# Kernel tuning notes

Measured on AMD Instinct MI355X. Metric: run time of the kernel, lower is better.

The kernel has to match this reference:

```python
import jax, jax.numpy as jnp
import numpy as np

N_NODES = 100000
N_EDGES = 1600000
IN_F = 32
D = 128
OUT = 16


def setup_inputs() -> dict:
    key = jax.random.key(0)
    ks = jax.random.split(key, 12)
    inp = {
        "x": jax.random.normal(ks[0], (N_NODES, IN_F), dtype=jnp.float32),
        "edge_index": jax.random.randint(ks[1], (2, N_EDGES), 0, N_NODES, dtype=jnp.int64),
        # node embedder (Linear IN_F -> D)
        "W_emb": jax.random.normal(ks[2], (IN_F, D), dtype=jnp.float32) / np.sqrt(IN_F),
        "b_emb": jnp.zeros((D,), dtype=jnp.float32),
        # conv1: relation weight, root weight, bias
        "W1_rel": jax.random.normal(ks[3], (D, D), dtype=jnp.float32) / np.sqrt(D),
        "W1_root": jax.random.normal(ks[4], (D, D), dtype=jnp.float32) / np.sqrt(D),
        "b1": jnp.zeros((D,), dtype=jnp.float32),
        # conv2
        "W2_rel": jax.random.normal(ks[5], (D, D), dtype=jnp.float32) / np.sqrt(D),
        "W2_root": jax.random.normal(ks[6], (D, D), dtype=jnp.float32) / np.sqrt(D),
        "b2": jnp.zeros((D,), dtype=jnp.float32),
        # final layer D -> OUT
        "W_out": jax.random.normal(ks[7], (D, OUT), dtype=jnp.float32) / np.sqrt(D),
        "b_out": jnp.zeros((OUT,), dtype=jnp.float32),
    }
    return inp


def _rgcn_mean(h, src, dst, W_rel, W_root, b):
    # FastRGCNConv with num_relations=1, aggr='mean':
    # out_i = mean_{j -> i}(h_j @ W_rel) + h_i @ W_root + b
    msg = h[src] @ W_rel  # [E, D] gather + per-edge transform
    agg = jax.ops.segment_sum(msg, dst, num_segments=N_NODES)
    cnt = jax.ops.segment_sum(jnp.ones((dst.shape[0],), dtype=h.dtype), dst,
                              num_segments=N_NODES)
    agg = agg / jnp.maximum(cnt, 1.0)[:, None]  # scatter-mean; isolated nodes -> 0
    return agg + h @ W_root + b


def reference(x, edge_index, W_emb, b_emb, W1_rel, W1_root, b1,
              W2_rel, W2_root, b2, W_out, b_out):
    src, dst = edge_index[0], edge_index[1]
    h = x @ W_emb + b_emb                                   # node embed
    h = jax.nn.relu(_rgcn_mean(h, src, dst, W1_rel, W1_root, b1))
    h = jax.nn.relu(_rgcn_mean(h, src, dst, W2_rel, W2_root, b2))
    return h @ W_out + b_out                                # [N_NODES, OUT]
```

## Files before the change

kernel.cpp:

```cpp
#include <hip/hip_runtime.h>
#include <hip/hip_bf16.h>

#define N_NODES 100000
#define N_EDGES 1600000
#define IN_F    32
#define D       128
#define OUT_F   16
#define NB      ((N_NODES + 255) / 256)
#define NSLICE  8
#define SLICE_NODES (N_NODES / NSLICE)
#define FILL_CHUNKS 512

typedef __attribute__((ext_vector_type(8))) short  bf16x8;
typedef __attribute__((ext_vector_type(4))) float  f32x4;

__device__ __forceinline__ unsigned short f2bf(float x) {
    unsigned u = __float_as_uint(x);
    unsigned r = (u + 0x7FFFu + ((u >> 16) & 1u)) >> 16;
    return (unsigned short)r;
}
__device__ __forceinline__ float bf2f(unsigned short h) {
    return __uint_as_float(((unsigned)h) << 16);
}

__global__ __launch_bounds__(256) void k_embed(const float* __restrict__ x,
                                               const float* __restrict__ W,
                                               const float* __restrict__ b,
                                               unsigned short* __restrict__ h_hi,
                                               unsigned short* __restrict__ h_lo) {
    __shared__ float xs[16][IN_F];
    const int base = blockIdx.x * 16;

    if (threadIdx.x < 128) {
        int r = threadIdx.x >> 3, c4 = (threadIdx.x & 7) << 2;
        *reinterpret_cast<float4*>(&xs[r][c4]) =
            *reinterpret_cast<const float4*>(x + (long)(base + r) * IN_F + c4);
    }
    __syncthreads();

    const int nl   = threadIdx.x >> 4;
    const int col0 = (threadIdx.x & 15) << 3;

    float acc[8];
    {
        float4 b0 = *reinterpret_cast<const float4*>(b + col0);
        float4 b1 = *reinterpret_cast<const float4*>(b + col0 + 4);
        acc[0] = b0.x; acc[1] = b0.y; acc[2] = b0.z; acc[3] = b0.w;
        acc[4] = b1.x; acc[5] = b1.y; acc[6] = b1.z; acc[7] = b1.w;
    }
#pragma unroll
    for (int k = 0; k < IN_F; ++k) {
        const float xv = xs[nl][k];
        float4 w0 = *reinterpret_cast<const float4*>(W + k * D + col0);
        float4 w1 = *reinterpret_cast<const float4*>(W + k * D + col0 + 4);
        acc[0] += xv * w0.x; acc[1] += xv * w0.y; acc[2] += xv * w0.z; acc[3] += xv * w0.w;
        acc[4] += xv * w1.x; acc[5] += xv * w1.y; acc[6] += xv * w1.z; acc[7] += xv * w1.w;
    }

    unsigned short hh[8], ll[8];
#pragma unroll
    for (int j = 0; j < 8; ++j) {
        unsigned short h = f2bf(acc[j]);
        hh[j] = h;
        ll[j] = f2bf(acc[j] - bf2f(h));
    }
    long off = (long)(base + nl) * D + col0;
    *reinterpret_cast<bf16x8*>(h_hi + off) = *reinterpret_cast<bf16x8*>(hh);
    *reinterpret_cast<bf16x8*>(h_lo + off) = *reinterpret_cast<bf16x8*>(ll);
}

__global__ __launch_bounds__(256) void k_count(const int* __restrict__ dst,
                                               int* __restrict__ cnt) {
    const int slice = blockIdx.x & (NSLICE - 1);
    const int chunk = blockIdx.x >> 3;
    const int lo = slice * SLICE_NODES;
    const int hi = lo + SLICE_NODES;
    for (int e = chunk * 256 + threadIdx.x; e < N_EDGES; e += FILL_CHUNKS * 256) {
        int d = dst[e];
        if (d >= lo && d < hi) atomicAdd(&cnt[d], 1);
    }
}

__global__ __launch_bounds__(256) void k_scan1(const int* __restrict__ cnt,
                                               int* __restrict__ part,
                                               int* __restrict__ blockSums) {
    __shared__ int s[256];
    int i = blockIdx.x * 256 + threadIdx.x;
    int v = (i < N_NODES) ? cnt[i] : 0;
    s[threadIdx.x] = v;
    __syncthreads();
    for (int off = 1; off < 256; off <<= 1) {
        int x = (threadIdx.x >= off) ? s[threadIdx.x - off] : 0;
        __syncthreads();
        s[threadIdx.x] += x;
        __syncthreads();
    }
    if (i < N_NODES) part[i] = s[threadIdx.x] - v;
    if (threadIdx.x == 255) blockSums[blockIdx.x] = s[255];
}

__global__ __launch_bounds__(512) void k_scan2(int* __restrict__ blockSums) {
    __shared__ int s[512];
    int t = threadIdx.x;
    int v = (t < NB) ? blockSums[t] : 0;
    s[t] = v;
    __syncthreads();
    for (int off = 1; off < 512; off <<= 1) {
        int x = (t >= off) ? s[t - off] : 0;
        __syncthreads();
        s[t] += x;
        __syncthreads();
    }
    if (t < NB) blockSums[t] = s[t] - v;
}

__global__ __launch_bounds__(256) void k_scan3(int* __restrict__ offsets,
                                               const int* __restrict__ blockSums,
                                               int* __restrict__ cursor) {
    int i = blockIdx.x * 256 + threadIdx.x;
    if (i < N_NODES) {
        int o = offsets[i] + blockSums[blockIdx.x];
        offsets[i] = o;
        cursor[i]  = o;
    }
}

__global__ __launch_bounds__(256) void k_fill(const int* __restrict__ src,
                                              const int* __restrict__ dst,
                                              int* __restrict__ cursor,
                                              int* __restrict__ csr) {
    const int slice = blockIdx.x & (NSLICE - 1);
    const int chunk = blockIdx.x >> 3;
    const int lo = slice * SLICE_NODES;
    const int hi = lo + SLICE_NODES;
    for (int e = chunk * 256 + threadIdx.x; e < N_EDGES; e += FILL_CHUNKS * 256) {
        int d = dst[e];
        if (d >= lo && d < hi) {
            int p = atomicAdd(&cursor[d], 1);
            csr[p] = src[e];
        }
    }
}

__global__ __launch_bounds__(256) void k_wprep(const float* __restrict__ W1r,
                                               const float* __restrict__ W1o,
                                               const float* __restrict__ W2r,
                                               const float* __restrict__ W2o,
                                               unsigned short* __restrict__ wp) {
    int c = blockIdx.x * 256 + threadIdx.x;
    int layer = c >> 12;
    int ko = (c >> 7) & 31;
    int n = c & 127;
    const float* Wrel  = layer ? W2r : W1r;
    const float* Wroot = layer ? W2o : W1o;

    unsigned short hi[8], lo[8];
#pragma unroll
    for (int j = 0; j < 8; ++j) {
        int k = ko * 8 + j;
        float w = (k < D) ? Wrel[k * D + n] : Wroot[(k - D) * D + n];
        unsigned short h = f2bf(w);
        hi[j] = h;
        lo[j] = f2bf(w - bf2f(h));
    }
    unsigned short* base = wp + layer * 65536 + ((ko * 128 + n) << 3);
    *reinterpret_cast<bf16x8*>(base)         = *reinterpret_cast<bf16x8*>(hi);
    *reinterpret_cast<bf16x8*>(base + 32768) = *reinterpret_cast<bf16x8*>(lo);
}

template <bool LAST>
__global__ __launch_bounds__(512) void k_fused(const unsigned short* __restrict__ hin_hi,
                                               const unsigned short* __restrict__ hin_lo,
                                               const int* __restrict__ csr,
                                               const int* __restrict__ offsets,
                                               const int* __restrict__ cnt,
                                               const unsigned short* __restrict__ Wh,
                                               const unsigned short* __restrict__ Wl,
                                               const float* __restrict__ b,
                                               unsigned short* __restrict__ ho_hi,
                                               unsigned short* __restrict__ ho_lo,
                                               const float* __restrict__ Wout,
                                               const float* __restrict__ bout,
                                               float* __restrict__ outp) {
    __shared__ unsigned short Ahi[32 * 32 * 8];
    __shared__ unsigned short Alo[32 * 32 * 8];
    const int base = blockIdx.x * 32;
    const int tid  = threadIdx.x;

    {
        const int ko  = tid & 15;
        const int q8  = ko << 3;
        const int row = tid >> 4;
        const int node = base + row;
        const int beg = offsets[node];
        const int deg = cnt[node];
        const int end = beg + deg;

        float a0[8], a1[8];
#pragma unroll
        for (int j = 0; j < 8; ++j) { a0[j] = 0.f; a1[j] = 0.f; }

        int i = beg;
        for (; i + 3 < end; i += 4) {
            int s0 = csr[i], s1 = csr[i + 1], s2 = csr[i + 2], s3 = csr[i + 3];
            bf16x8 v0 = *reinterpret_cast<const bf16x8*>(hin_hi + (long)s0 * D + q8);
            bf16x8 v1 = *reinterpret_cast<const bf16x8*>(hin_hi + (long)s1 * D + q8);
            bf16x8 v2 = *reinterpret_cast<const bf16x8*>(hin_hi + (long)s2 * D + q8);
            bf16x8 v3 = *reinterpret_cast<const bf16x8*>(hin_hi + (long)s3 * D + q8);
#pragma unroll
            for (int j = 0; j < 8; ++j) {
                a0[j] += bf2f((unsigned short)v0[j]) + bf2f((unsigned short)v1[j]);
                a1[j] += bf2f((unsigned short)v2[j]) + bf2f((unsigned short)v3[j]);
            }
        }
        for (; i < end; ++i) {
            int s0 = csr[i];
            bf16x8 v0 = *reinterpret_cast<const bf16x8*>(hin_hi + (long)s0 * D + q8);
#pragma unroll
            for (int j = 0; j < 8; ++j) a0[j] += bf2f((unsigned short)v0[j]);
        }

        const float sc = 1.f / fmaxf((float)deg, 1.f);
        unsigned short hh[8], ll[8];
#pragma unroll
        for (int j = 0; j < 8; ++j) {
            float v = (a0[j] + a1[j]) * sc;
            unsigned short h = f2bf(v);
            hh[j] = h;
            ll[j] = f2bf(v - bf2f(h));
        }
        const int byteoff = ((ko * 32 + row) * 16) ^ ((ko & 7) << 4);
        *reinterpret_cast<bf16x8*>(reinterpret_cast<char*>(Ahi) + byteoff) =
            *reinterpret_cast<bf16x8*>(hh);
        *reinterpret_cast<bf16x8*>(reinterpret_cast<char*>(Alo) + byteoff) =
            *reinterpret_cast<bf16x8*>(ll);
    }

    {
        int ko16 = tid & 15;
        int row  = tid >> 4;
        long off = (long)(base + row) * D + ko16 * 8;
        bf16x8 vh = *reinterpret_cast<const bf16x8*>(hin_hi + off);
        bf16x8 vl = *reinterpret_cast<const bf16x8*>(hin_lo + off);
        int ko = 16 + ko16;
        int byteoff = ((ko * 32 + row) * 16) ^ ((ko & 7) << 4);
        *reinterpret_cast<bf16x8*>(reinterpret_cast<char*>(Ahi) + byteoff) = vh;
        *reinterpret_cast<bf16x8*>(reinterpret_cast<char*>(Alo) + byteoff) = vl;
    }
    __syncthreads();

    const int lane = tid & 63;
    const int wid  = tid >> 6;
    const int mw  = wid & 1;
    const int nwq = wid >> 1;
    const int l15 = lane & 15;
    const int l4  = lane >> 4;

    f32x4 acc[2];
#pragma unroll
    for (int ct = 0; ct < 2; ++ct) acc[ct] = (f32x4){0.f, 0.f, 0.f, 0.f};

    const int arow = mw * 16 + l15;

#pragma unroll
    for (int s = 0; s < 8; ++s) {
        const int ks = s * 4 + l4;
        const int abyte = ((ks * 32 + arow) * 16) ^ ((ks & 7) << 4);
        bf16x8 ah = *reinterpret_cast<const bf16x8*>(
                        reinterpret_cast<const char*>(Ahi) + abyte);
        bf16x8 al = *reinterpret_cast<const bf16x8*>(
                        reinterpret_cast<const char*>(Alo) + abyte);
#pragma unroll
        for (int ct = 0; ct < 2; ++ct) {
            const int colb = nwq * 32 + ct * 16 + l15;
            const long bidx = ((long)(ks * 128 + colb)) << 3;
            bf16x8 bh = *reinterpret_cast<const bf16x8*>(Wh + bidx);
            bf16x8 bl = *reinterpret_cast<const bf16x8*>(Wl + bidx);
            acc[ct] = __builtin_amdgcn_mfma_f32_16x16x32_bf16(ah, bh, acc[ct], 0, 0, 0);
            acc[ct] = __builtin_amdgcn_mfma_f32_16x16x32_bf16(al, bh, acc[ct], 0, 0, 0);
            acc[ct] = __builtin_amdgcn_mfma_f32_16x16x32_bf16(ah, bl, acc[ct], 0, 0, 0);
        }
    }

    if (!LAST) {
#pragma unroll
        for (int ct = 0; ct < 2; ++ct) {
            const int col = nwq * 32 + ct * 16 + l15;
            const float bv = b[col];
#pragma unroll
            for (int r = 0; r < 4; ++r) {
                long node = base + mw * 16 + l4 * 4 + r;
                float v = fmaxf(acc[ct][r] + bv, 0.f);
                unsigned short h = f2bf(v);
                ho_hi[node * D + col] = h;
                ho_lo[node * D + col] = f2bf(v - bf2f(h));
            }
        }
    } else {
        __syncthreads();
        float* hsm = reinterpret_cast<float*>(Ahi);
#pragma unroll
        for (int ct = 0; ct < 2; ++ct) {
            const int col = nwq * 32 + ct * 16 + l15;
            const float bv = b[col];
#pragma unroll
            for (int r = 0; r < 4; ++r) {
                int nl = mw * 16 + l4 * 4 + r;
                hsm[nl * D + ((col + 4 * nl) & 127)] = fmaxf(acc[ct][r] + bv, 0.f);
            }
        }
        __syncthreads();

        const int nl = tid >> 4;
        const int oo = tid & 15;
        float acc0 = bout[oo];
#pragma unroll 8
        for (int k = 0; k < D; ++k) {
            float hv = hsm[nl * D + ((k + 4 * nl) & 127)];
            acc0 += hv * Wout[k * OUT_F + oo];
        }
        outp[(long)(base + nl) * OUT_F + oo] = acc0;
    }
}

extern "C" void kernel_launch(void* const* d_in, const int* in_sizes, int n_in,
                              void* d_out, int out_size, void* d_ws, size_t ws_size,
                              hipStream_t stream) {
    const float* x      = (const float*)d_in[0];
    const int*   edge   = (const int*)d_in[1];
    const float* W_emb  = (const float*)d_in[2];
    const float* b_emb  = (const float*)d_in[3];
    const float* W1_rel = (const float*)d_in[4];
    const float* W1_root= (const float*)d_in[5];
    const float* b1     = (const float*)d_in[6];
    const float* W2_rel = (const float*)d_in[7];
    const float* W2_root= (const float*)d_in[8];
    const float* b2     = (const float*)d_in[9];
    const float* W_out  = (const float*)d_in[10];
    const float* b_out  = (const float*)d_in[11];
    float* out = (float*)d_out;

    const int* src = edge;
    const int* dst = edge + N_EDGES;

    const size_t ND = (size_t)N_NODES * D;

    unsigned short* hA_hi = (unsigned short*)d_ws;
    unsigned short* hA_lo = hA_hi + ND;
    unsigned short* hB_hi = hA_lo + ND;
    unsigned short* hB_lo = hB_hi + ND;
    int*   cnt     = (int*)(hB_lo + ND);
    int*   offsets = cnt + N_NODES;
    int*   cursor  = offsets + N_NODES;
    int*   bsums   = cursor + N_NODES;
    unsigned short* wpack = (unsigned short*)(bsums + 400);
    int*   csr     = (int*)(wpack + 4 * 32768);

    hipMemsetAsync(cnt, 0, N_NODES * sizeof(int), stream);
    k_count<<<NSLICE * FILL_CHUNKS, 256, 0, stream>>>(dst, cnt);
    k_scan1<<<NB, 256, 0, stream>>>(cnt, offsets, bsums);
    k_scan2<<<1, 512, 0, stream>>>(bsums);
    k_scan3<<<NB, 256, 0, stream>>>(offsets, bsums, cursor);
    k_fill<<<NSLICE * FILL_CHUNKS, 256, 0, stream>>>(src, dst, cursor, csr);
    k_wprep<<<32, 256, 0, stream>>>(W1_rel, W1_root, W2_rel, W2_root, wpack);

    k_embed<<<N_NODES / 16, 256, 0, stream>>>(x, W_emb, b_emb, hA_hi, hA_lo);

    k_fused<false><<<N_NODES / 32, 512, 0, stream>>>(
        hA_hi, hA_lo, csr, offsets, cnt,
        wpack, wpack + 32768, b1, hB_hi, hB_lo, nullptr, nullptr, nullptr);

    k_fused<true><<<N_NODES / 32, 512, 0, stream>>>(
        hB_hi, hB_lo, csr, offsets, cnt,
        wpack + 65536, wpack + 98304, b2, nullptr, nullptr, W_out, b_out, out);
}
```

Measured before the change: 460.9 us.

## Merge embed, count and weight-prep kernels; vectorize edge loads; software-pipeline gather

```diff
diff --git a/kernel.cpp b/kernel.cpp
--- a/kernel.cpp
+++ b/kernel.cpp
@@ -9,7 +9,12 @@
 #define NB      ((N_NODES + 255) / 256)
 #define NSLICE  8
 #define SLICE_NODES (N_NODES / NSLICE)
-#define FILL_CHUNKS 512
+
+#define NI4     (N_EDGES / 4)
+#define EBLK    ((NI4 + 1023) / 1024)
+#define NEMB    (N_NODES / 16)
+#define NCNT    (NSLICE * EBLK)
+#define NWP     32
 
 typedef __attribute__((ext_vector_type(8))) short  bf16x8;
 typedef __attribute__((ext_vector_type(4))) float  f32x4;
@@ -23,61 +28,107 @@
     return __uint_as_float(((unsigned)h) << 16);
 }
 
-__global__ __launch_bounds__(256) void k_embed(const float* __restrict__ x,
-                                               const float* __restrict__ W,
-                                               const float* __restrict__ b,
-                                               unsigned short* __restrict__ h_hi,
-                                               unsigned short* __restrict__ h_lo) {
-    __shared__ float xs[16][IN_F];
-    const int base = blockIdx.x * 16;
-
-    if (threadIdx.x < 128) {
-        int r = threadIdx.x >> 3, c4 = (threadIdx.x & 7) << 2;
-        *reinterpret_cast<float4*>(&xs[r][c4]) =
-            *reinterpret_cast<const float4*>(x + (long)(base + r) * IN_F + c4);
-    }
-    __syncthreads();
-
-    const int nl   = threadIdx.x >> 4;
-    const int col0 = (threadIdx.x & 15) << 3;
-
-    float acc[8];
-    {
-        float4 b0 = *reinterpret_cast<const float4*>(b + col0);
-        float4 b1 = *reinterpret_cast<const float4*>(b + col0 + 4);
-        acc[0] = b0.x; acc[1] = b0.y; acc[2] = b0.z; acc[3] = b0.w;
-        acc[4] = b1.x; acc[5] = b1.y; acc[6] = b1.z; acc[7] = b1.w;
-    }
-#pragma unroll
-    for (int k = 0; k < IN_F; ++k) {
-        const float xv = xs[nl][k];
-        float4 w0 = *reinterpret_cast<const float4*>(W + k * D + col0);
-        float4 w1 = *reinterpret_cast<const float4*>(W + k * D + col0 + 4);
-        acc[0] += xv * w0.x; acc[1] += xv * w0.y; acc[2] += xv * w0.z; acc[3] += xv * w0.w;
-        acc[4] += xv * w1.x; acc[5] += xv * w1.y; acc[6] += xv * w1.z; acc[7] += xv * w1.w;
-    }
-
-    unsigned short hh[8], ll[8];
-#pragma unroll
-    for (int j = 0; j < 8; ++j) {
-        unsigned short h = f2bf(acc[j]);
-        hh[j] = h;
-        ll[j] = f2bf(acc[j] - bf2f(h));
-    }
-    long off = (long)(base + nl) * D + col0;
-    *reinterpret_cast<bf16x8*>(h_hi + off) = *reinterpret_cast<bf16x8*>(hh);
-    *reinterpret_cast<bf16x8*>(h_lo + off) = *reinterpret_cast<bf16x8*>(ll);
-}
-
-__global__ __launch_bounds__(256) void k_count(const int* __restrict__ dst,
-                                               int* __restrict__ cnt) {
-    const int slice = blockIdx.x & (NSLICE - 1);
-    const int chunk = blockIdx.x >> 3;
-    const int lo = slice * SLICE_NODES;
-    const int hi = lo + SLICE_NODES;
-    for (int e = chunk * 256 + threadIdx.x; e < N_EDGES; e += FILL_CHUNKS * 256) {
-        int d = dst[e];
-        if (d >= lo && d < hi) atomicAdd(&cnt[d], 1);
+__global__ __launch_bounds__(256) void k_prep(const float* __restrict__ x,
+                                              const float* __restrict__ Wemb,
+                                              const float* __restrict__ bemb,
+                                              unsigned short* __restrict__ h_hi,
+                                              unsigned short* __restrict__ h_lo,
+                                              const int* __restrict__ dst,
+                                              int* __restrict__ cnt,
+                                              const float* __restrict__ W1r,
+                                              const float* __restrict__ W1o,
+                                              const float* __restrict__ W2r,
+                                              const float* __restrict__ W2o,
+                                              unsigned short* __restrict__ wp) {
+    const int bid = blockIdx.x;
+    const int tid = threadIdx.x;
+
+    if (bid < NEMB) {
+        __shared__ float xs[16][IN_F];
+        const int base = bid * 16;
+        if (tid < 128) {
+            int r = tid >> 3, c4 = (tid & 7) << 2;
+            *reinterpret_cast<float4*>(&xs[r][c4]) =
+                *reinterpret_cast<const float4*>(x + (long)(base + r) * IN_F + c4);
+        }
+        __syncthreads();
+
+        const int nl   = tid >> 4;
+        const int col0 = (tid & 15) << 3;
+
+        float acc[8];
+        {
+            float4 b0 = *reinterpret_cast<const float4*>(bemb + col0);
+            float4 b1 = *reinterpret_cast<const float4*>(bemb + col0 + 4);
+            acc[0] = b0.x; acc[1] = b0.y; acc[2] = b0.z; acc[3] = b0.w;
+            acc[4] = b1.x; acc[5] = b1.y; acc[6] = b1.z; acc[7] = b1.w;
+        }
+#pragma unroll
+        for (int k = 0; k < IN_F; ++k) {
+            const float xv = xs[nl][k];
+            float4 w0 = *reinterpret_cast<const float4*>(Wemb + k * D + col0);
+            float4 w1 = *reinterpret_cast<const float4*>(Wemb + k * D + col0 + 4);
+            acc[0] += xv * w0.x; acc[1] += xv * w0.y; acc[2] += xv * w0.z; acc[3] += xv * w0.w;
+            acc[4] += xv * w1.x; acc[5] += xv * w1.y; acc[6] += xv * w1.z; acc[7] += xv * w1.w;
+        }
+        unsigned short hh[8], ll[8];
+#pragma unroll
+        for (int j = 0; j < 8; ++j) {
+            unsigned short h = f2bf(acc[j]);
+            hh[j] = h;
+            ll[j] = f2bf(acc[j] - bf2f(h));
+        }
+        long off = (long)(base + nl) * D + col0;
+        *reinterpret_cast<bf16x8*>(h_hi + off) = *reinterpret_cast<bf16x8*>(hh);
+        *reinterpret_cast<bf16x8*>(h_lo + off) = *reinterpret_cast<bf16x8*>(ll);
+
+    } else if (bid < NEMB + NCNT) {
+        const int cb    = bid - NEMB;
+        const int slice = cb & (NSLICE - 1);
+        const int chunk = cb >> 3;
+        const int lo = slice * SLICE_NODES;
+        const int hi = lo + SLICE_NODES;
+        const int4* dst4 = reinterpret_cast<const int4*>(dst);
+        const int i4base = chunk * 1024;
+
+        int4 d[4];
+        bool ok[4];
+#pragma unroll
+        for (int j = 0; j < 4; ++j) {
+            int idx = i4base + j * 256 + tid;
+            ok[j] = idx < NI4;
+            if (ok[j]) d[j] = dst4[idx];
+        }
+#pragma unroll
+        for (int j = 0; j < 4; ++j) {
+            if (ok[j]) {
+                if (d[j].x >= lo && d[j].x < hi) atomicAdd(&cnt[d[j].x], 1);
+                if (d[j].y >= lo && d[j].y < hi) atomicAdd(&cnt[d[j].y], 1);
+                if (d[j].z >= lo && d[j].z < hi) atomicAdd(&cnt[d[j].z], 1);
+                if (d[j].w >= lo && d[j].w < hi) atomicAdd(&cnt[d[j].w], 1);
+            }
+        }
+
+    } else {
+        int c = (bid - NEMB - NCNT) * 256 + tid;
+        int layer = c >> 12;
+        int ko = (c >> 7) & 31;
+        int n = c & 127;
+        const float* Wrel  = layer ? W2r : W1r;
+        const float* Wroot = layer ? W2o : W1o;
+
+        unsigned short hi8[8], lo8[8];
+#pragma unroll
+        for (int j = 0; j < 8; ++j) {
+            int k = ko * 8 + j;
+            float w = (k < D) ? Wrel[k * D + n] : Wroot[(k - D) * D + n];
+            unsigned short h = f2bf(w);
+            hi8[j] = h;
+            lo8[j] = f2bf(w - bf2f(h));
+        }
+        unsigned short* base = wp + layer * 65536 + ((ko * 128 + n) << 3);
+        *reinterpret_cast<bf16x8*>(base)         = *reinterpret_cast<bf16x8*>(hi8);
+        *reinterpret_cast<bf16x8*>(base + 32768) = *reinterpret_cast<bf16x8*>(lo8);
     }
 }
 
@@ -133,39 +184,28 @@
     const int chunk = blockIdx.x >> 3;
     const int lo = slice * SLICE_NODES;
     const int hi = lo + SLICE_NODES;
-    for (int e = chunk * 256 + threadIdx.x; e < N_EDGES; e += FILL_CHUNKS * 256) {
-        int d = dst[e];
-        if (d >= lo && d < hi) {
-            int p = atomicAdd(&cursor[d], 1);
-            csr[p] = src[e];
-        }
-    }
-}
-
-__global__ __launch_bounds__(256) void k_wprep(const float* __restrict__ W1r,
-                                               const float* __restrict__ W1o,
-                                               const float* __restrict__ W2r,
-                                               const float* __restrict__ W2o,
-                                               unsigned short* __restrict__ wp) {
-    int c = blockIdx.x * 256 + threadIdx.x;
-    int layer = c >> 12;
-    int ko = (c >> 7) & 31;
-    int n = c & 127;
-    const float* Wrel  = layer ? W2r : W1r;
-    const float* Wroot = layer ? W2o : W1o;
-
-    unsigned short hi[8], lo[8];
-#pragma unroll
-    for (int j = 0; j < 8; ++j) {
-        int k = ko * 8 + j;
-        float w = (k < D) ? Wrel[k * D + n] : Wroot[(k - D) * D + n];
-        unsigned short h = f2bf(w);
-        hi[j] = h;
-        lo[j] = f2bf(w - bf2f(h));
-    }
-    unsigned short* base = wp + layer * 65536 + ((ko * 128 + n) << 3);
-    *reinterpret_cast<bf16x8*>(base)         = *reinterpret_cast<bf16x8*>(hi);
-    *reinterpret_cast<bf16x8*>(base + 32768) = *reinterpret_cast<bf16x8*>(lo);
+    const int4* dst4 = reinterpret_cast<const int4*>(dst);
+    const int4* src4 = reinterpret_cast<const int4*>(src);
+    const int i4base = chunk * 1024;
+    const int tid = threadIdx.x;
+
+    int4 d[4], s[4];
+    bool ok[4];
+#pragma unroll
+    for (int j = 0; j < 4; ++j) {
+        int idx = i4base + j * 256 + tid;
+        ok[j] = idx < NI4;
+        if (ok[j]) { d[j] = dst4[idx]; s[j] = src4[idx]; }
+    }
+#pragma unroll
+    for (int j = 0; j < 4; ++j) {
+        if (ok[j]) {
+            if (d[j].x >= lo && d[j].x < hi) { int p = atomicAdd(&cursor[d[j].x], 1); csr[p] = s[j].x; }
+            if (d[j].y >= lo && d[j].y < hi) { int p = atomicAdd(&cursor[d[j].y], 1); csr[p] = s[j].y; }
+            if (d[j].z >= lo && d[j].z < hi) { int p = atomicAdd(&cursor[d[j].z], 1); csr[p] = s[j].z; }
+            if (d[j].w >= lo && d[j].w < hi) { int p = atomicAdd(&cursor[d[j].w], 1); csr[p] = s[j].w; }
+        }
+    }
 }
 
 template <bool LAST>
@@ -201,16 +241,31 @@
         for (int j = 0; j < 8; ++j) { a0[j] = 0.f; a1[j] = 0.f; }
 
         int i = beg;
-        for (; i + 3 < end; i += 4) {
+        const int stop = beg + (deg & ~3);
+        if (i < stop) {
             int s0 = csr[i], s1 = csr[i + 1], s2 = csr[i + 2], s3 = csr[i + 3];
-            bf16x8 v0 = *reinterpret_cast<const bf16x8*>(hin_hi + (long)s0 * D + q8);
-            bf16x8 v1 = *reinterpret_cast<const bf16x8*>(hin_hi + (long)s1 * D + q8);
-            bf16x8 v2 = *reinterpret_cast<const bf16x8*>(hin_hi + (long)s2 * D + q8);
-            bf16x8 v3 = *reinterpret_cast<const bf16x8*>(hin_hi + (long)s3 * D + q8);
+            bf16x8 p0 = *reinterpret_cast<const bf16x8*>(hin_hi + (long)s0 * D + q8);
+            bf16x8 p1 = *reinterpret_cast<const bf16x8*>(hin_hi + (long)s1 * D + q8);
+            bf16x8 p2 = *reinterpret_cast<const bf16x8*>(hin_hi + (long)s2 * D + q8);
+            bf16x8 p3 = *reinterpret_cast<const bf16x8*>(hin_hi + (long)s3 * D + q8);
+            i += 4;
+            for (; i < stop; i += 4) {
+                int t0 = csr[i], t1 = csr[i + 1], t2 = csr[i + 2], t3 = csr[i + 3];
+                bf16x8 n0 = *reinterpret_cast<const bf16x8*>(hin_hi + (long)t0 * D + q8);
+                bf16x8 n1 = *reinterpret_cast<const bf16x8*>(hin_hi + (long)t1 * D + q8);
+                bf16x8 n2 = *reinterpret_cast<const bf16x8*>(hin_hi + (long)t2 * D + q8);
+                bf16x8 n3 = *reinterpret_cast<const bf16x8*>(hin_hi + (long)t3 * D + q8);
+#pragma unroll
+                for (int j = 0; j < 8; ++j) {
+                    a0[j] += bf2f((unsigned short)p0[j]) + bf2f((unsigned short)p1[j]);
+                    a1[j] += bf2f((unsigned short)p2[j]) + bf2f((unsigned short)p3[j]);
+                }
+                p0 = n0; p1 = n1; p2 = n2; p3 = n3;
+            }
 #pragma unroll
             for (int j = 0; j < 8; ++j) {
-                a0[j] += bf2f((unsigned short)v0[j]) + bf2f((unsigned short)v1[j]);
-                a1[j] += bf2f((unsigned short)v2[j]) + bf2f((unsigned short)v3[j]);
+                a0[j] += bf2f((unsigned short)p0[j]) + bf2f((unsigned short)p1[j]);
+                a1[j] += bf2f((unsigned short)p2[j]) + bf2f((unsigned short)p3[j]);
             }
         }
         for (; i < end; ++i) {
@@ -357,14 +412,15 @@
     int*   csr     = (int*)(wpack + 4 * 32768);
 
     hipMemsetAsync(cnt, 0, N_NODES * sizeof(int), stream);
-    k_count<<<NSLICE * FILL_CHUNKS, 256, 0, stream>>>(dst, cnt);
+    k_prep<<<NEMB + NCNT + NWP, 256, 0, stream>>>(
+        x, W_emb, b_emb, hA_hi, hA_lo,
+        dst, cnt,
+        W1_rel, W1_root, W2_rel, W2_root, wpack);
+
     k_scan1<<<NB, 256, 0, stream>>>(cnt, offsets, bsums);
     k_scan2<<<1, 512, 0, stream>>>(bsums);
     k_scan3<<<NB, 256, 0, stream>>>(offsets, bsums, cursor);
-    k_fill<<<NSLICE * FILL_CHUNKS, 256, 0, stream>>>(src, dst, cursor, csr);
-    k_wprep<<<32, 256, 0, stream>>>(W1_rel, W1_root, W2_rel, W2_root, wpack);
-
-    k_embed<<<N_NODES / 16, 256, 0, stream>>>(x, W_emb, b_emb, hA_hi, hA_lo);
+    k_fill<<<NCNT, 256, 0, stream>>>(src, dst, cursor, csr);
 
     k_fused<false><<<N_NODES / 32, 512, 0, stream>>>(
         hA_hi, hA_lo, csr, offsets, cnt,
```

Result: slower. 473.1 us (+2.6%).
